# Performance work log

Measured on AMD Instinct MI355X. Metric: run time of the kernel, lower is better.

The kernel has to match this reference:

```python
import jax, jax.numpy as jnp
import numpy as np

OBJ_VD = 4096  # obj_config['visual_d']


def _forward3(x, Wh, bh, We, be):
    # HypernymVisual_acc.forward3 (dropout is identity in eval)
    x = jax.nn.relu(x)
    h = jax.nn.relu(x @ Wh.T + bh)
    return h @ We.T + be


def _po_sim(hypers, hypos):
    # PartialOrderSimilarity with p=2: -||relu(hypers - hypos)||_2 over last axis
    d = jax.nn.relu(hypers - hypos)
    return -jnp.sqrt(jnp.sum(d * d, axis=-1))


def setup_inputs() -> dict:
    key = jax.random.key(0)
    ks = jax.random.split(key, 18)
    B, NNEG, V, ED = 1024, 128, 100, 600
    s = 0.02
    return {
        "vfs": jax.random.normal(ks[0], (B, 12288), jnp.float32),
        "label_vecs": jax.random.normal(ks[1], (V, ED), jnp.float32),
        "pls": jax.random.randint(ks[2], (B,), 0, V),
        "nls": jax.random.randint(ks[3], (B, NNEG), 0, V),
        "W_h1": jax.random.normal(ks[4], (2048, 4096), jnp.float32) * s,
        "b_h1": jax.random.normal(ks[5], (2048,), jnp.float32) * s,
        "W_e1": jax.random.normal(ks[6], (600, 2048), jnp.float32) * s,
        "b_e1": jax.random.normal(ks[7], (600,), jnp.float32) * s,
        "W_h2": jax.random.normal(ks[8], (4096, 12288), jnp.float32) * s,
        "b_h2": jax.random.normal(ks[9], (4096,), jnp.float32) * s,
        "W_e2": jax.random.normal(ks[10], (600, 4096), jnp.float32) * s,
        "b_e2": jax.random.normal(ks[11], (600,), jnp.float32) * s,
        "W_h": jax.random.normal(ks[12], (1800, 1800), jnp.float32) * s,
        "b_h": jax.random.normal(ks[13], (1800,), jnp.float32) * s,
        "W_e": jax.random.normal(ks[14], (600, 1800), jnp.float32) * s,
        "b_e": jax.random.normal(ks[15], (600,), jnp.float32) * s,
    }


def reference(vfs, label_vecs, pls, nls,
              W_h1, b_h1, W_e1, b_e1,
              W_h2, b_h2, W_e2, b_e2,
              W_h, b_h, W_e, b_e):
    # PredicateVisual_acc.forward1 (dropout as eval identity)
    sbj = _forward3(vfs[:, :OBJ_VD], W_h1, b_h1, W_e1, b_e1)   # [B, 600]
    obj = _forward3(vfs[:, -OBJ_VD:], W_h1, b_h1, W_e1, b_e1)  # [B, 600]
    pre = _forward3(vfs, W_h2, b_h2, W_e2, b_e2)               # [B, 600]
    z = jnp.concatenate([sbj, pre, obj], axis=1)               # [B, 1800]
    z = jax.nn.relu(z)
    h = jax.nn.relu(z @ W_h.T + b_h)                           # [B, 1800]
    emb = h @ W_e.T + b_e                                      # [B, 600]
    p_scores = _po_sim(label_vecs[pls], emb)                   # [B]
    n_scores = _po_sim(label_vecs[nls], emb[:, None, :])       # [B, NNEG]
    return jnp.concatenate([p_scores[:, None], n_scores], axis=1)
```

## Files before the change

kernel.cpp:

```cpp
#include <hip/hip_runtime.h>
#include <hip/hip_bf16.h>

using f32x4  = __attribute__((ext_vector_type(4))) float;
using bf16x8 = __attribute__((ext_vector_type(8))) __bf16;

typedef const __attribute__((address_space(1))) unsigned int GU32;
typedef __attribute__((address_space(3))) unsigned int LU32;

__device__ __forceinline__ void gload_lds16(void* l, const void* g) {
    __builtin_amdgcn_global_load_lds((GU32*)g, (LU32*)l, 16, 0, 0);
}

template <int TM, int RELU, int BF16OUT, int PARTIAL>
__device__ __forceinline__ void gemm_body(
    bf16x8* As, bf16x8* Ws,
    const __bf16* __restrict__ A, int lda, long long a2_off, int msplit,
    const __bf16* __restrict__ Wt, int ldw, int wrows,
    const float* __restrict__ bias,
    void* __restrict__ Cout, int ldc, long long c2_off,
    int N, int K, int m0, int n0, int kb0, int ke, int zslice)
{
    constexpr int NIT = TM / 32;
    constexpr int FR  = TM / 32;
    const int t = threadIdx.x, l = t & 63, w = t >> 6;

    const __bf16* Ab = A + ((m0 >= msplit) ? a2_off : 0);
    const __bf16* asrc[NIT];
    const __bf16* wsrc[NIT];
    int dslot[NIT];
#pragma unroll
    for (int it = 0; it < NIT; ++it) {
        int slot = (w * NIT + it) * 64 + l;
        int kg   = slot / TM;
        int row  = slot % TM;
        asrc[it] = Ab + (size_t)(m0 + row) * lda + kg * 8 + kb0;
        int wrow = n0 + row; if (wrow >= wrows) wrow = wrows - 1;
        wsrc[it] = Wt + (size_t)wrow * ldw + kg * 8 + kb0;
        dslot[it] = (w * NIT + it) * 64;
    }

    const int lr = l & 15, lkg = l >> 4;
    const int wr = (w >> 1) * (TM / 2), wc = (w & 1) * (TM / 2);

    f32x4 acc[FR][FR] = {};

    for (int kb = kb0; kb < ke; kb += 64) {
#pragma unroll
        for (int it = 0; it < NIT; ++it) {
            gload_lds16(&As[dslot[it]], asrc[it]);
            gload_lds16(&Ws[dslot[it]], wsrc[it]);
            asrc[it] += 64; wsrc[it] += 64;
        }
        __syncthreads();
#pragma unroll
        for (int ks = 0; ks < 2; ++ks) {
            const int kgf = ks * 4 + lkg;
            bf16x8 af[FR], wf[FR];
#pragma unroll
            for (int m = 0; m < FR; ++m) af[m] = As[kgf * TM + wr + m * 16 + lr];
#pragma unroll
            for (int n = 0; n < FR; ++n) wf[n] = Ws[kgf * TM + wc + n * 16 + lr];
#pragma unroll
            for (int m = 0; m < FR; ++m)
#pragma unroll
                for (int n = 0; n < FR; ++n)
                    acc[m][n] = __builtin_amdgcn_mfma_f32_16x16x32_bf16(
                        af[m], wf[n], acc[m][n], 0, 0, 0);
        }
        __syncthreads();
    }

    const long long coff = PARTIAL ? (long long)zslice * c2_off
                                   : ((m0 >= msplit) ? c2_off : 0);
#pragma unroll
    for (int n = 0; n < FR; ++n) {
        int col = n0 + wc + n * 16 + lr;
        if (col >= N) continue;
        float bv = PARTIAL ? 0.f : bias[col];
#pragma unroll
        for (int m = 0; m < FR; ++m) {
            int rbase = m0 + wr + m * 16 + lkg * 4;
#pragma unroll
            for (int j = 0; j < 4; ++j) {
                long long idx = (long long)(rbase + j) * ldc + col + coff;
                if (PARTIAL) {
                    ((float*)Cout)[idx] = acc[m][n][j];
                } else {
                    float v = acc[m][n][j] + bv;
                    if (RELU) v = fmaxf(v, 0.f);
                    if (BF16OUT) ((__bf16*)Cout)[idx] = (__bf16)v;
                    else         ((float*)Cout)[idx]  = v;
                }
            }
        }
    }
}

template <int RELU, int BF16OUT, int PARTIAL>
__global__ __launch_bounds__(256)
void gemm128(const __bf16* __restrict__ A, int lda, long long a2_off, int msplit,
             const __bf16* __restrict__ Wt, int ldw, int wrows,
             const float* __restrict__ bias,
             void* __restrict__ Cout, int ldc, long long c2_off,
             int N, int K, int kchunk)
{
    __shared__ bf16x8 As[1024];
    __shared__ bf16x8 Ws[1024];
    int kb0 = blockIdx.z * kchunk;
    int ke  = min(kb0 + kchunk, K);
    gemm_body<128, RELU, BF16OUT, PARTIAL>(
        As, Ws, A, lda, a2_off, msplit, Wt, ldw, wrows, bias,
        Cout, ldc, c2_off, N, K, blockIdx.y << 7, blockIdx.x << 7,
        kb0, ke, blockIdx.z);
}

struct GDesc {
    const __bf16* A; const __bf16* W; const float* bias; void* out;
    long long a2, c2;
    int lda, ldw, wrows, ldc, N, K, ntx, msplit;
};

template <int RELU, int BF16OUT>
__global__ __launch_bounds__(256)
void gemm64_dual(GDesc d0, GDesc d1, int nblk0)
{
    __shared__ bf16x8 As[512];
    __shared__ bf16x8 Ws[512];
    int bid = blockIdx.x;
    GDesc d = (bid < nblk0) ? d0 : d1;
    int tid = (bid < nblk0) ? bid : bid - nblk0;
    int tx = tid % d.ntx, ty = tid / d.ntx;
    gemm_body<64, RELU, BF16OUT, 0>(
        As, Ws, d.A, d.lda, d.a2, d.msplit, d.W, d.ldw, d.wrows, d.bias,
        d.out, d.ldc, d.c2, d.N, d.K, ty << 6, tx << 6, 0, d.K, 0);
}

template <int RELU, int BF16OUT>
__global__ __launch_bounds__(256)
void reduce_k(const float* __restrict__ part, long long zs, int S,
              const float* __restrict__ bias, void* __restrict__ out,
              int N, int ldc, int msplit, long long c2, int M)
{
    const int n8 = N >> 3;
    const long long total = (long long)M * n8;
    for (long long i = (long long)blockIdx.x * 256 + threadIdx.x; i < total;
         i += (long long)gridDim.x * 256) {
        int row = (int)(i / n8);
        int c8  = (int)(i - (long long)row * n8) << 3;
        long long base = (long long)row * N + c8;
        float4 s0 = {0.f, 0.f, 0.f, 0.f}, s1 = {0.f, 0.f, 0.f, 0.f};
        for (int s = 0; s < S; ++s) {
            const float4* p = (const float4*)(part + s * zs + base);
            float4 a = p[0], b = p[1];
            s0.x += a.x; s0.y += a.y; s0.z += a.z; s0.w += a.w;
            s1.x += b.x; s1.y += b.y; s1.z += b.z; s1.w += b.w;
        }
        float v[8] = {s0.x, s0.y, s0.z, s0.w, s1.x, s1.y, s1.z, s1.w};
        long long ob = (long long)row * ldc + c8 + ((row >= msplit) ? c2 : 0);
        if (BF16OUT) {
            bf16x8 o;
#pragma unroll
            for (int j = 0; j < 8; ++j) {
                float x = v[j] + bias[c8 + j];
                if (RELU) x = fmaxf(x, 0.f);
                o[j] = (__bf16)x;
            }
            *(bf16x8*)((__bf16*)out + ob) = o;
        } else {
            float t0[8];
#pragma unroll
            for (int j = 0; j < 8; ++j) {
                float x = v[j] + bias[c8 + j];
                if (RELU) x = fmaxf(x, 0.f);
                t0[j] = x;
            }
            float4 o0 = {t0[0], t0[1], t0[2], t0[3]};
            float4 o1 = {t0[4], t0[5], t0[6], t0[7]};
            *(float4*)((float*)out + ob)     = o0;
            *(float4*)((float*)out + ob + 4) = o1;
        }
    }
}

__global__ __launch_bounds__(256)
void conv_bf16(const float* __restrict__ in, __bf16* __restrict__ out,
               long long n, int relu)
{
    long long stride = (long long)gridDim.x * 256 * 8;
    for (long long i = ((long long)blockIdx.x * 256 + threadIdx.x) * 8; i < n; i += stride) {
        float4 f0 = *(const float4*)(in + i);
        float4 f1 = *(const float4*)(in + i + 4);
        float v[8] = {f0.x, f0.y, f0.z, f0.w, f1.x, f1.y, f1.z, f1.w};
        bf16x8 o;
#pragma unroll
        for (int j = 0; j < 8; ++j) {
            float x = v[j];
            if (relu) x = fmaxf(x, 0.f);
            o[j] = (__bf16)x;
        }
        *(bf16x8*)(out + i) = o;
    }
}

__global__ __launch_bounds__(256)
void conv_pad(const float* __restrict__ in, __bf16* __restrict__ out,
              int rows, int cols, int ldo)
{
    int v8 = ldo >> 3;
    long long total = (long long)rows * v8;
    for (long long s = (long long)blockIdx.x * 256 + threadIdx.x; s < total;
         s += (long long)gridDim.x * 256) {
        int r  = (int)(s / v8);
        int c8 = ((int)(s % v8)) << 3;
        bf16x8 o;
        if (c8 + 8 <= cols) {
            const float* p = in + (size_t)r * cols + c8;
            float4 f0 = *(const float4*)p;
            float4 f1 = *(const float4*)(p + 4);
            float v[8] = {f0.x, f0.y, f0.z, f0.w, f1.x, f1.y, f1.z, f1.w};
#pragma unroll
            for (int j = 0; j < 8; ++j) o[j] = (__bf16)v[j];
        } else {
#pragma unroll
            for (int j = 0; j < 8; ++j) o[j] = (__bf16)0.f;
        }
        *(bf16x8*)(out + (size_t)r * ldo + c8) = o;
    }
}

__global__ __launch_bounds__(256)
void zero_cols(__bf16* __restrict__ buf, int rows, int c0, int ld)
{
    int wpad = ld - c0;
    int total = rows * wpad;
    for (int i = blockIdx.x * 256 + threadIdx.x; i < total; i += gridDim.x * 256)
        buf[(size_t)(i / wpad) * ld + c0 + (i % wpad)] = (__bf16)0.f;
}

__global__ __launch_bounds__(256)
void score_kernel(const float* __restrict__ emb,
                  const float* __restrict__ labels,
                  const int* __restrict__ pls,
                  const int* __restrict__ nls,
                  float* __restrict__ out)
{
    const int b = blockIdx.x;
    __shared__ float e[600];
    for (int i = threadIdx.x; i < 600; i += 256) e[i] = emb[(size_t)b * 600 + i];
    __syncthreads();

    const int w = threadIdx.x >> 6;
    const int lane = threadIdx.x & 63;
    for (int j = w; j < 129; j += 4) {
        int idx = (j == 0) ? pls[b] : nls[(size_t)b * 128 + (j - 1)];
        const float* lv = labels + (size_t)idx * 600;
        float s = 0.f;
        for (int d = lane; d < 600; d += 64) {
            float df = lv[d] - e[d];
            df = fmaxf(df, 0.f);
            s += df * df;
        }
#pragma unroll
        for (int off = 32; off >= 1; off >>= 1) s += __shfl_xor(s, off, 64);
        if (lane == 0) out[(size_t)b * 129 + j] = -sqrtf(s);
    }
}

extern "C" void kernel_launch(void* const* d_in, const int* in_sizes, int n_in,
                              void* d_out, int out_size, void* d_ws, size_t ws_size,
                              hipStream_t stream)
{
    const float* vfs    = (const float*)d_in[0];
    const float* labels = (const float*)d_in[1];
    const int*   pls    = (const int*)d_in[2];
    const int*   nls    = (const int*)d_in[3];
    const float* W_h1   = (const float*)d_in[4];
    const float* b_h1   = (const float*)d_in[5];
    const float* W_e1   = (const float*)d_in[6];
    const float* b_e1   = (const float*)d_in[7];
    const float* W_h2   = (const float*)d_in[8];
    const float* b_h2   = (const float*)d_in[9];
    const float* W_e2   = (const float*)d_in[10];
    const float* b_e2   = (const float*)d_in[11];
    const float* W_h    = (const float*)d_in[12];
    const float* b_h    = (const float*)d_in[13];
    const float* W_e    = (const float*)d_in[14];
    const float* b_e    = (const float*)d_in[15];

    char* p = (char*)d_ws;
    auto alloc = [&](size_t bytes) { char* r = p; p += (bytes + 255) & ~size_t(255); return r; };
    __bf16* vfs_bf = (__bf16*)alloc(1024ll * 12288 * 2);
    __bf16* h1     = (__bf16*)alloc(2048ll * 2048 * 2);
    __bf16* hp     = (__bf16*)alloc(1024ll * 4096 * 2);
    __bf16* z      = (__bf16*)alloc(1024ll * 1856 * 2);
    __bf16* h2     = (__bf16*)alloc(1024ll * 1856 * 2);
    float*  emb    = (float*)alloc(1024ll * 600 * 4);
    __bf16* Wh1b   = (__bf16*)alloc(2048ll * 4096 * 2);
    __bf16* Wh2b   = (__bf16*)alloc(4096ll * 12288 * 2);
    __bf16* We1b   = (__bf16*)alloc(600ll * 2048 * 2);
    __bf16* We2b   = (__bf16*)alloc(600ll * 4096 * 2);
    __bf16* Whb    = (__bf16*)alloc(1800ll * 1856 * 2);
    __bf16* Web    = (__bf16*)alloc(600ll * 1856 * 2);

    size_t used  = (size_t)(p - (char*)d_ws);
    size_t rem   = (ws_size > used) ? (ws_size - used) : 0;
    size_t arena = rem > (64u << 20) ? (64u << 20) : (rem & ~size_t(255));
    float* part  = (float*)alloc(arena);

    dim3 blk(256);
    const int HUGE_SPLIT = 1 << 30;

    auto pickS = [&](int M, int N, int smax) {
        int s = smax;
        while (s > 1 && (long long)s * M * N * 4 > (long long)arena) s >>= 1;
        return s;
    };
    auto gemm = [&](const __bf16* A, int lda, long long a2, int msA,
                    const __bf16* W, int ldw, int wrows, const float* bias,
                    void* out, int ldc, int msC, long long c2,
                    int M, int N, int K, int smax) {
        int S = pickS(M, N, smax);
        int nx = (N + 127) >> 7, ny = M >> 7;
        if (S == 1) {
            gemm128<1, 1, 0><<<dim3(nx, ny, 1), blk, 0, stream>>>(
                A, lda, a2, (msA == HUGE_SPLIT ? msC : msA), W, ldw, wrows,
                bias, out, ldc, c2, N, K, K);
        } else {
            int kchunk = (((K + S - 1) / S) + 63) & ~63;
            long long zs = (long long)M * N;
            gemm128<0, 0, 1><<<dim3(nx, ny, S), blk, 0, stream>>>(
                A, lda, a2, msA, W, ldw, wrows, nullptr,
                part, N, zs, N, K, kchunk);
            long long tot8 = (long long)M * (N >> 3);
            int rblocks = (int)((tot8 + 255) / 256);
            if (rblocks > 2048) rblocks = 2048;
            reduce_k<1, 1><<<dim3(rblocks), blk, 0, stream>>>(
                part, zs, S, bias, out, N, ldc, msC, c2, M);
        }
    };

    conv_bf16<<<2048, blk, 0, stream>>>(vfs, vfs_bf, 1024ll * 12288, 1);
    conv_bf16<<<1024, blk, 0, stream>>>(W_h1, Wh1b, 2048ll * 4096, 0);
    conv_bf16<<<2048, blk, 0, stream>>>(W_h2, Wh2b, 4096ll * 12288, 0);
    conv_bf16<<<512,  blk, 0, stream>>>(W_e1, We1b, 600ll * 2048, 0);
    conv_bf16<<<512,  blk, 0, stream>>>(W_e2, We2b, 600ll * 4096, 0);
    conv_pad<<<1024, blk, 0, stream>>>(W_h, Whb, 1800, 1800, 1856);
    conv_pad<<<512,  blk, 0, stream>>>(W_e, Web, 600, 1800, 1856);
    zero_cols<<<256, blk, 0, stream>>>(z,  1024, 1800, 1856);
    zero_cols<<<256, blk, 0, stream>>>(h2, 1024, 1800, 1856);

    gemm(vfs_bf, 12288, 8192ll - 1024ll * 12288, 1024,
         Wh1b, 4096, 2048, b_h1, h1, 2048, HUGE_SPLIT, 0,
         2048, 2048, 4096, 4);
    gemm(vfs_bf, 12288, 0, HUGE_SPLIT,
         Wh2b, 12288, 4096, b_h2, hp, 4096, HUGE_SPLIT, 0,
         1024, 4096, 12288, 4);

    {
        GDesc d3{h1,  We1b, b_e1, z,       0, 1200ll - 1024ll * 1856,
                 2048, 2048, 600, 1856, 600, 2048, 10, 1024};
        GDesc d4{hp,  We2b, b_e2, z + 600, 0, 0,
                 4096, 4096, 600, 1856, 600, 4096, 10, HUGE_SPLIT};
        gemm64_dual<1, 1><<<dim3(480), blk, 0, stream>>>(d3, d4, 320);
    }
    {
        GDesc d5{z, Whb, b_h, h2, 0, 0,
                 1856, 1856, 1800, 1856, 1800, 1856, 29, HUGE_SPLIT};
        gemm64_dual<1, 1><<<dim3(464), blk, 0, stream>>>(d5, d5, 464);
    }
    {
        GDesc d6{h2, Web, b_e, emb, 0, 0,
                 1856, 1856, 600, 600, 600, 1856, 10, HUGE_SPLIT};
        gemm64_dual<0, 0><<<dim3(160), blk, 0, stream>>>(d6, d6, 160);
    }

    score_kernel<<<dim3(1024), blk, 0, stream>>>(emb, labels, pls, nls, (float*)d_out);
}
```

Baseline: 952.2 us.

## Add 256x256 double-buffered split-K GEMM kernel for the two large projections

Adds a new 512-thread GEMM kernel with 256x256 output tiles and a two-stage LDS double buffer fed by direct global-to-LDS loads. It replaces the 128x128 split-K kernel for the two large hidden-layer GEMMs when the shapes are multiples of 256. Larger tiles raise arithmetic intensity and cut redundant global loads, and the double buffer overlaps loads with MFMA work. The cost is fewer blocks and heavier register and LDS use per block (128 KB LDS, 128 accumulator floats per thread), which could hurt occupancy or spill.

```diff
diff --git a/kernel.cpp b/kernel.cpp
--- a/kernel.cpp
+++ b/kernel.cpp
@@ -9,6 +9,114 @@
 
 __device__ __forceinline__ void gload_lds16(void* l, const void* g) {
     __builtin_amdgcn_global_load_lds((GU32*)g, (LU32*)l, 16, 0, 0);
+}
+
+template <int RELU, int BF16OUT, int PARTIAL>
+__global__ __launch_bounds__(512)
+void gemm256_2ph(const __bf16* __restrict__ A, int lda, long long a2_off, int msplit,
+                 const __bf16* __restrict__ Wt, int ldw, int wrows,
+                 const float* __restrict__ bias,
+                 void* __restrict__ Cout, int ldc, long long c2_off,
+                 int N, int K, int kchunk)
+{
+    __shared__ bf16x8 As[2][2048];
+    __shared__ bf16x8 Ws[2][2048];
+
+    const int t = threadIdx.x, l = t & 63, w = t >> 6;
+    const int m0 = blockIdx.y << 8;
+    const int n0 = blockIdx.x << 8;
+    const int kb0 = blockIdx.z * kchunk;
+    const int NT  = (min(kb0 + kchunk, K) - kb0) >> 6;
+
+    const __bf16* Ab = A + ((m0 >= msplit) ? a2_off : 0);
+
+    const __bf16* asrc[4];
+    const __bf16* wsrc[4];
+    int dbase[4];
+#pragma unroll
+    for (int it = 0; it < 4; ++it) {
+        int slot = it * 512 + t;
+        int kg = slot >> 8, row = slot & 255;
+        asrc[it] = Ab + (size_t)(m0 + row) * lda + kg * 8 + kb0;
+        int wrow = n0 + row; if (wrow >= wrows) wrow = wrows - 1;
+        wsrc[it] = Wt + (size_t)wrow * ldw + kg * 8 + kb0;
+        dbase[it] = it * 512 + w * 64;
+    }
+
+    auto stage = [&](int buf, int koff) {
+#pragma unroll
+        for (int it = 0; it < 4; ++it)
+            gload_lds16(&As[buf][dbase[it]], asrc[it] + koff);
+#pragma unroll
+        for (int it = 0; it < 4; ++it)
+            gload_lds16(&Ws[buf][dbase[it]], wsrc[it] + koff);
+    };
+
+    const int lr = l & 15, lkg = l >> 4;
+    const int wr = (w >> 2) << 7;
+    const int wc = (w & 3) << 6;
+
+    f32x4 acc[8][4] = {};
+
+    stage(0, 0);
+    if (NT > 1) stage(1, 64);
+
+    for (int tt = 0; tt < NT; ++tt) {
+        if (tt + 1 < NT) asm volatile("s_waitcnt vmcnt(8)" ::: "memory");
+        else             asm volatile("s_waitcnt vmcnt(0)" ::: "memory");
+        __builtin_amdgcn_sched_barrier(0);
+        __builtin_amdgcn_s_barrier();
+        __builtin_amdgcn_sched_barrier(0);
+
+        const bf16x8* Al = As[tt & 1];
+        const bf16x8* Wl = Ws[tt & 1];
+#pragma unroll
+        for (int ks = 0; ks < 2; ++ks) {
+            const int kgf = ks * 4 + lkg;
+            bf16x8 af[8], wf[4];
+#pragma unroll
+            for (int m = 0; m < 8; ++m) af[m] = Al[kgf * 256 + wr + m * 16 + lr];
+#pragma unroll
+            for (int n = 0; n < 4; ++n) wf[n] = Wl[kgf * 256 + wc + n * 16 + lr];
+#pragma unroll
+            for (int m = 0; m < 8; ++m)
+#pragma unroll
+                for (int n = 0; n < 4; ++n)
+                    acc[m][n] = __builtin_amdgcn_mfma_f32_16x16x32_bf16(
+                        af[m], wf[n], acc[m][n], 0, 0, 0);
+        }
+
+        asm volatile("s_waitcnt lgkmcnt(0)" ::: "memory");
+        __builtin_amdgcn_sched_barrier(0);
+        __builtin_amdgcn_s_barrier();
+        __builtin_amdgcn_sched_barrier(0);
+        if (tt + 2 < NT) stage(tt & 1, (tt + 2) << 6);
+    }
+
+    const long long coff = PARTIAL ? (long long)blockIdx.z * c2_off
+                                   : ((m0 >= msplit) ? c2_off : 0);
+#pragma unroll
+    for (int n = 0; n < 4; ++n) {
+        int col = n0 + wc + n * 16 + lr;
+        if (col >= N) continue;
+        float bv = PARTIAL ? 0.f : bias[col];
+#pragma unroll
+        for (int m = 0; m < 8; ++m) {
+            int rbase = m0 + wr + m * 16 + lkg * 4;
+#pragma unroll
+            for (int j = 0; j < 4; ++j) {
+                long long idx = (long long)(rbase + j) * ldc + col + coff;
+                if (PARTIAL) {
+                    ((float*)Cout)[idx] = acc[m][n][j];
+                } else {
+                    float v = acc[m][n][j] + bv;
+                    if (RELU) v = fmaxf(v, 0.f);
+                    if (BF16OUT) ((__bf16*)Cout)[idx] = (__bf16)v;
+                    else         ((float*)Cout)[idx]  = v;
+                }
+            }
+        }
+    }
 }
 
 template <int TM, int RELU, int BF16OUT, int PARTIAL>
@@ -315,20 +423,15 @@
         while (s > 1 && (long long)s * M * N * 4 > (long long)arena) s >>= 1;
         return s;
     };
-    auto gemm = [&](const __bf16* A, int lda, long long a2, int msA,
-                    const __bf16* W, int ldw, int wrows, const float* bias,
-                    void* out, int ldc, int msC, long long c2,
-                    int M, int N, int K, int smax) {
+    auto gemmBig = [&](const __bf16* A, int lda, long long a2, int msA,
+                       const __bf16* W, int ldw, int wrows, const float* bias,
+                       void* out, int ldc, int msC, long long c2,
+                       int M, int N, int K, int smax) {
         int S = pickS(M, N, smax);
-        int nx = (N + 127) >> 7, ny = M >> 7;
-        if (S == 1) {
-            gemm128<1, 1, 0><<<dim3(nx, ny, 1), blk, 0, stream>>>(
-                A, lda, a2, (msA == HUGE_SPLIT ? msC : msA), W, ldw, wrows,
-                bias, out, ldc, c2, N, K, K);
-        } else {
+        if (S >= 2 && (M % 256) == 0 && (N % 256) == 0) {
             int kchunk = (((K + S - 1) / S) + 63) & ~63;
             long long zs = (long long)M * N;
-            gemm128<0, 0, 1><<<dim3(nx, ny, S), blk, 0, stream>>>(
+            gemm256_2ph<0, 0, 1><<<dim3(N >> 8, M >> 8, S), dim3(512), 0, stream>>>(
                 A, lda, a2, msA, W, ldw, wrows, nullptr,
                 part, N, zs, N, K, kchunk);
             long long tot8 = (long long)M * (N >> 3);
@@ -336,6 +439,10 @@
             if (rblocks > 2048) rblocks = 2048;
             reduce_k<1, 1><<<dim3(rblocks), blk, 0, stream>>>(
                 part, zs, S, bias, out, N, ldc, msC, c2, M);
+        } else {
+            gemm128<1, 1, 0><<<dim3((N + 127) >> 7, M >> 7, 1), blk, 0, stream>>>(
+                A, lda, a2, (msA == HUGE_SPLIT ? msC : msA), W, ldw, wrows,
+                bias, out, ldc, c2, N, K, K);
         }
     };
 
@@ -349,12 +456,12 @@
     zero_cols<<<256, blk, 0, stream>>>(z,  1024, 1800, 1856);
     zero_cols<<<256, blk, 0, stream>>>(h2, 1024, 1800, 1856);
 
-    gemm(vfs_bf, 12288, 8192ll - 1024ll * 12288, 1024,
-         Wh1b, 4096, 2048, b_h1, h1, 2048, HUGE_SPLIT, 0,
-         2048, 2048, 4096, 4);
-    gemm(vfs_bf, 12288, 0, HUGE_SPLIT,
-         Wh2b, 12288, 4096, b_h2, hp, 4096, HUGE_SPLIT, 0,
-         1024, 4096, 12288, 4);
+    gemmBig(vfs_bf, 12288, 8192ll - 1024ll * 12288, 1024,
+            Wh1b, 4096, 2048, b_h1, h1, 2048, HUGE_SPLIT, 0,
+            2048, 2048, 4096, 4);
+    gemmBig(vfs_bf, 12288, 0, HUGE_SPLIT,
+            Wh2b, 12288, 4096, b_h2, hp, 4096, HUGE_SPLIT, 0,
+            1024, 4096, 12288, 4);
 
     {
         GDesc d3{h1,  We1b, b_e1, z,       0, 1200ll - 1024ll * 1856,
```

Result: faster. 877.0 us (-7.9%).
